# Performance work log

Hardware: AMD Instinct MI355X
Metric: run time of the kernel (lower is better)

## Reference

```python
import jax, jax.numpy as jnp
import numpy as np

B, C, H, W = 2, 64, 512, 896


def setup_inputs() -> dict:
    key = jax.random.key(0)
    k1, k2 = jax.random.split(key)
    feature = jax.random.normal(k1, (B, C, H, W), dtype=jnp.float32)
    # flow in pixel units; a few pixels of motion is typical for video frames
    flow = jax.random.normal(k2, (B, 2, H, W), dtype=jnp.float32) * 3.0
    return {"feature": feature, "flow": flow}


def reference(feature, flow):
    # Flownet2-style Resample2d: out[b,c,y,x] = bilinear(feature[b,c], y+v, x+u)
    # with zero contribution from out-of-bounds taps.
    Bv, Cv, Hv, Wv = feature.shape
    HW = Hv * Wv
    gx = flow[:, 0] + jnp.arange(Wv, dtype=flow.dtype)[None, None, :]  # [B,H,W]
    gy = flow[:, 1] + jnp.arange(Hv, dtype=flow.dtype)[None, :, None]  # [B,H,W]
    x0f = jnp.floor(gx)
    y0f = jnp.floor(gy)
    wx = gx - x0f  # frac weights
    wy = gy - y0f
    x0 = x0f.astype(jnp.int32)
    y0 = y0f.astype(jnp.int32)
    feat = feature.reshape(Bv, Cv, HW)

    def corner(xi, yi, w):
        # zero out-of-bounds taps; clip indices so the gather is always legal
        valid = (xi >= 0) & (xi < Wv) & (yi >= 0) & (yi < Hv)
        idx = jnp.clip(yi, 0, Hv - 1) * Wv + jnp.clip(xi, 0, Wv - 1)  # [B,H,W]
        idx = jnp.broadcast_to(idx.reshape(Bv, 1, HW), (Bv, Cv, HW))
        v = jnp.take_along_axis(feat, idx, axis=2)  # [B,C,HW]
        wm = (w * valid.astype(w.dtype)).reshape(Bv, 1, HW)
        return v * wm

    out = (
        corner(x0, y0, (1.0 - wx) * (1.0 - wy))
        + corner(x0 + 1, y0, wx * (1.0 - wy))
        + corner(x0, y0 + 1, (1.0 - wx) * wy)
        + corner(x0 + 1, y0 + 1, wx * wy)
    )
    return out.reshape(Bv, Cv, Hv, Wv)
```

## Files before the change

kernel.cpp:

```cpp
#include <hip/hip_runtime.h>


#define Bv 2
#define Cv 64
#define Hv 512
#define Wv 896
#define HWsz (Hv * Wv)

#define TILE 64
#define CPB 4
#define NCG (Cv / CPB)
#define SW 90
#define SH 88
#define XOFF 12
#define YOFF 11
#define NSITES (SH * SW)
#define NTX (Wv / TILE)
#define NTY (Hv / TILE)
#define NTILES (NTX * NTY)
#define NBLK (Bv * NCG * NTILES)
#define THREADS 1024
#define NW (THREADS / 64)
#define KITERS (TILE * TILE / THREADS)
#define LDS_BYTES (NSITES * CPB * 4)

__global__ __launch_bounds__(THREADS) void resample2d_kernel(
    const float* __restrict__ feature,
    const float* __restrict__ flow,
    float* __restrict__ out) {
    extern __shared__ float smem[];

    const int orig = blockIdx.x;
    const int wid = (orig & 7) * (NBLK / 8) + (orig >> 3);
    const int txi = wid % NTX;
    const int t2 = wid / NTX;
    const int tyi = t2 % NTY;
    const int zb = t2 / NTY;
    const int b = zb / NCG;
    const int c0 = (zb % NCG) * CPB;

    const int tx0 = txi * TILE;
    const int ty0 = tyi * TILE;
    const int xs = tx0 - XOFF;
    const int ys = ty0 - YOFF;

    const int tid = threadIdx.x;
    const int lane = tid & 63;
    const int wv = tid >> 6;

    const float* __restrict__ fbase = feature + ((size_t)b * Cv + c0) * HWsz;
    const float* __restrict__ flb = flow + (size_t)b * 2 * HWsz;
    float* __restrict__ ob = out + ((size_t)b * Cv + c0) * HWsz;

    const int px = tx0 + lane;
    float u[KITERS], v[KITERS];
    int pixk[KITERS];
#pragma unroll
    for (int k = 0; k < KITERS; ++k) {
        const int y = ty0 + wv + NW * k;
        pixk[k] = y * Wv + px;
        u[k] = flb[pixk[k]];
        v[k] = flb[HWsz + pixk[k]];
    }

    const bool interior = (xs >= 0) & (xs + SW <= Wv) & (ys >= 0) & (ys + SH <= Hv);
    if (interior) {
#pragma unroll
        for (int k = 0; k < 8; ++k) {
            const int p = tid + THREADS * k;
            if (p < NSITES) {
                const int r = p / SW;
                const int xx = p - r * SW;
                const float* src = fbase + (size_t)(ys + r) * Wv + (xs + xx);
                float4 val;
                val.x = src[0];
                val.y = src[HWsz];
                val.z = src[2 * HWsz];
                val.w = src[3 * HWsz];
                *(float4*)(&smem[(size_t)p * CPB]) = val;
            }
        }
    } else {
#pragma unroll
        for (int k = 0; k < 8; ++k) {
            const int p = tid + THREADS * k;
            if (p < NSITES) {
                const int r = p / SW;
                const int xx = p - r * SW;
                const int gy = ys + r;
                const int gx = xs + xx;
                float4 val = make_float4(0.0f, 0.0f, 0.0f, 0.0f);
                if (((unsigned)gy < (unsigned)Hv) & ((unsigned)gx < (unsigned)Wv)) {
                    const float* src = fbase + (size_t)gy * Wv + gx;
                    val.x = src[0];
                    val.y = src[HWsz];
                    val.z = src[2 * HWsz];
                    val.w = src[3 * HWsz];
                }
                *(float4*)(&smem[(size_t)p * CPB]) = val;
            }
        }
    }

    float w00[KITERS], w10[KITERS], w01[KITERS], w11[KITERS];
    int ac[KITERS];
    bool inwin[KITERS];
#pragma unroll
    for (int k = 0; k < KITERS; ++k) {
        const int y = ty0 + wv + NW * k;
        const float gx = u[k] + (float)px;
        const float gy = v[k] + (float)y;
        const float x0f = floorf(gx);
        const float y0f = floorf(gy);
        const float wx = gx - x0f;
        const float wy = gy - y0f;
        const float omx = 1.0f - wx;
        const float omy = 1.0f - wy;
        w00[k] = omx * omy;
        w10[k] = wx * omy;
        w01[k] = omx * wy;
        w11[k] = wx * wy;
        const int lx = (int)x0f - xs;
        const int ly = (int)y0f - ys;
        inwin[k] = ((unsigned)lx <= (unsigned)(SW - 2)) &
                   ((unsigned)ly <= (unsigned)(SH - 2));
        const int lxc = min(max(lx, 0), SW - 2);
        const int lyc = min(max(ly, 0), SH - 2);
        ac[k] = (lyc * SW + lxc) * CPB;
    }

    __syncthreads();

#define READ(T, K)                                                  \
    do {                                                            \
        const int a_ = ac[K];                                       \
        T[0] = *(const float4*)(&smem[a_]);                         \
        T[1] = *(const float4*)(&smem[a_ + CPB]);                   \
        T[2] = *(const float4*)(&smem[a_ + SW * CPB]);              \
        T[3] = *(const float4*)(&smem[a_ + SW * CPB + CPB]);        \
    } while (0)

#define CONSUME(T, K)                                                         \
    do {                                                                      \
        if (!inwin[K]) {     \
            const float gx_ = u[K] + (float)px;                               \
            const float gy_ = v[K] + (float)(ty0 + wv + NW * (K));            \
            const int x0_ = (int)floorf(gx_);                                 \
            const int y0_ = (int)floorf(gy_);                                 \
            const int x1_ = x0_ + 1, y1_ = y0_ + 1;                           \
            const bool vx0 = (unsigned)x0_ < (unsigned)Wv;                    \
            const bool vx1 = (unsigned)x1_ < (unsigned)Wv;                    \
            const bool vy0 = (unsigned)y0_ < (unsigned)Hv;                    \
            const bool vy1 = (unsigned)y1_ < (unsigned)Hv;                    \
            const int cx0 = min(max(x0_, 0), Wv - 1);                         \
            const int cx1 = min(max(x1_, 0), Wv - 1);                         \
            const int cy0 = min(max(y0_, 0), Hv - 1);                         \
            const int cy1 = min(max(y1_, 0), Hv - 1);                         \
            _Pragma("unroll") for (int c = 0; c < CPB; ++c) {                 \
                const float* f = fbase + (size_t)c * HWsz;                    \
                ((float*)&T[0])[c] = (vx0 & vy0) ? f[cy0 * Wv + cx0] : 0.0f;  \
                ((float*)&T[1])[c] = (vx1 & vy0) ? f[cy0 * Wv + cx1] : 0.0f;  \
                ((float*)&T[2])[c] = (vx0 & vy1) ? f[cy1 * Wv + cx0] : 0.0f;  \
                ((float*)&T[3])[c] = (vx1 & vy1) ? f[cy1 * Wv + cx1] : 0.0f;  \
            }                                                                 \
        }                                                                     \
        _Pragma("unroll") for (int c = 0; c < CPB; ++c) {                     \
            const float r_ = ((const float*)&T[0])[c] * w00[K] +              \
                             ((const float*)&T[1])[c] * w10[K] +              \
                             ((const float*)&T[2])[c] * w01[K] +              \
                             ((const float*)&T[3])[c] * w11[K];               \
            __builtin_nontemporal_store(r_, &ob[(size_t)c * HWsz + pixk[K]]); \
        }                                                                     \
    } while (0)

    float4 tA[4], tB[4];
    READ(tA, 0);
    READ(tB, 1);
    CONSUME(tA, 0);
    READ(tA, 2);
    CONSUME(tB, 1);
    READ(tB, 3);
    CONSUME(tA, 2);
    CONSUME(tB, 3);

#undef READ
#undef CONSUME
}

extern "C" void kernel_launch(void* const* d_in, const int* in_sizes, int n_in,
                              void* d_out, int out_size, void* d_ws, size_t ws_size,
                              hipStream_t stream) {
    const float* feature = (const float*)d_in[0];
    const float* flow = (const float*)d_in[1];
    float* out = (float*)d_out;

    static bool inited = false;
    if (!inited) {
        hipFuncSetAttribute((const void*)resample2d_kernel,
                            hipFuncAttributeMaxDynamicSharedMemorySize, LDS_BYTES);
        inited = true;
    }

    dim3 block(THREADS, 1, 1);
    dim3 grid(NBLK, 1, 1);
    resample2d_kernel<<<grid, block, LDS_BYTES, stream>>>(feature, flow, out);
}
```

Before: 467.6 us.

## Halve channels per block to shrink LDS tile and raise occupancy

Cuts channels per block from four to two, so the LDS halo tile is stored as float2 in static shared memory and each block needs half the LDS. The launch bound now asks for a minimum of 8 blocks, which pressures the compiler to cut registers. Bilinear weights are computed at consume time from wx/wy, and in-window flags are packed into a bitmask. The goal is more resident waves to hide gather and load latency. The cost is twice as many blocks, each reloading flow and recomputing coordinates and halo, and the padded stride becomes 91.

```diff
diff --git a/kernel.cpp b/kernel.cpp
--- a/kernel.cpp
+++ b/kernel.cpp
@@ -8,9 +8,9 @@
 #define HWsz (Hv * Wv)
 
 #define TILE 64
-#define CPB 4
+#define CPB 2
 #define NCG (Cv / CPB)
-#define SW 90
+#define SW 91
 #define SH 88
 #define XOFF 12
 #define YOFF 11
@@ -22,13 +22,12 @@
 #define THREADS 1024
 #define NW (THREADS / 64)
 #define KITERS (TILE * TILE / THREADS)
-#define LDS_BYTES (NSITES * CPB * 4)
 
-__global__ __launch_bounds__(THREADS) void resample2d_kernel(
+__global__ __launch_bounds__(THREADS, 8) void resample2d_kernel(
     const float* __restrict__ feature,
     const float* __restrict__ flow,
     float* __restrict__ out) {
-    extern __shared__ float smem[];
+    __shared__ float2 smem[NSITES];
 
     const int orig = blockIdx.x;
     const int wid = (orig & 7) * (NBLK / 8) + (orig >> 3);
@@ -54,13 +53,12 @@
 
     const int px = tx0 + lane;
     float u[KITERS], v[KITERS];
-    int pixk[KITERS];
 #pragma unroll
     for (int k = 0; k < KITERS; ++k) {
         const int y = ty0 + wv + NW * k;
-        pixk[k] = y * Wv + px;
-        u[k] = flb[pixk[k]];
-        v[k] = flb[HWsz + pixk[k]];
+        const int pix = y * Wv + px;
+        u[k] = flb[pix];
+        v[k] = flb[HWsz + pix];
     }
 
     const bool interior = (xs >= 0) & (xs + SW <= Wv) & (ys >= 0) & (ys + SH <= Hv);
@@ -72,12 +70,10 @@
                 const int r = p / SW;
                 const int xx = p - r * SW;
                 const float* src = fbase + (size_t)(ys + r) * Wv + (xs + xx);
-                float4 val;
+                float2 val;
                 val.x = src[0];
                 val.y = src[HWsz];
-                val.z = src[2 * HWsz];
-                val.w = src[3 * HWsz];
-                *(float4*)(&smem[(size_t)p * CPB]) = val;
+                smem[p] = val;
             }
         }
     } else {
@@ -89,22 +85,20 @@
                 const int xx = p - r * SW;
                 const int gy = ys + r;
                 const int gx = xs + xx;
-                float4 val = make_float4(0.0f, 0.0f, 0.0f, 0.0f);
+                float2 val = make_float2(0.0f, 0.0f);
                 if (((unsigned)gy < (unsigned)Hv) & ((unsigned)gx < (unsigned)Wv)) {
                     const float* src = fbase + (size_t)gy * Wv + gx;
                     val.x = src[0];
                     val.y = src[HWsz];
-                    val.z = src[2 * HWsz];
-                    val.w = src[3 * HWsz];
                 }
-                *(float4*)(&smem[(size_t)p * CPB]) = val;
+                smem[p] = val;
             }
         }
     }
 
-    float w00[KITERS], w10[KITERS], w01[KITERS], w11[KITERS];
+    float wx[KITERS], wy[KITERS];
     int ac[KITERS];
-    bool inwin[KITERS];
+    unsigned iw = 0;
 #pragma unroll
     for (int k = 0; k < KITERS; ++k) {
         const int y = ty0 + wv + NW * k;
@@ -112,68 +106,70 @@
         const float gy = v[k] + (float)y;
         const float x0f = floorf(gx);
         const float y0f = floorf(gy);
-        const float wx = gx - x0f;
-        const float wy = gy - y0f;
-        const float omx = 1.0f - wx;
-        const float omy = 1.0f - wy;
-        w00[k] = omx * omy;
-        w10[k] = wx * omy;
-        w01[k] = omx * wy;
-        w11[k] = wx * wy;
+        wx[k] = gx - x0f;
+        wy[k] = gy - y0f;
         const int lx = (int)x0f - xs;
         const int ly = (int)y0f - ys;
-        inwin[k] = ((unsigned)lx <= (unsigned)(SW - 2)) &
-                   ((unsigned)ly <= (unsigned)(SH - 2));
+        const bool inwin = ((unsigned)lx <= (unsigned)(SW - 2)) &
+                           ((unsigned)ly <= (unsigned)(SH - 2));
+        iw |= inwin ? (1u << k) : 0u;
         const int lxc = min(max(lx, 0), SW - 2);
         const int lyc = min(max(ly, 0), SH - 2);
-        ac[k] = (lyc * SW + lxc) * CPB;
+        ac[k] = lyc * SW + lxc;
     }
 
     __syncthreads();
 
-#define READ(T, K)                                                  \
-    do {                                                            \
-        const int a_ = ac[K];                                       \
-        T[0] = *(const float4*)(&smem[a_]);                         \
-        T[1] = *(const float4*)(&smem[a_ + CPB]);                   \
-        T[2] = *(const float4*)(&smem[a_ + SW * CPB]);              \
-        T[3] = *(const float4*)(&smem[a_ + SW * CPB + CPB]);        \
+#define READ(T, K)                        \
+    do {                                  \
+        const int a_ = ac[K];             \
+        T[0] = smem[a_];                  \
+        T[1] = smem[a_ + 1];              \
+        T[2] = smem[a_ + SW];             \
+        T[3] = smem[a_ + SW + 1];         \
     } while (0)
 
-#define CONSUME(T, K)                                                         \
-    do {                                                                      \
-        if (!inwin[K]) {     \
-            const float gx_ = u[K] + (float)px;                               \
-            const float gy_ = v[K] + (float)(ty0 + wv + NW * (K));            \
-            const int x0_ = (int)floorf(gx_);                                 \
-            const int y0_ = (int)floorf(gy_);                                 \
-            const int x1_ = x0_ + 1, y1_ = y0_ + 1;                           \
-            const bool vx0 = (unsigned)x0_ < (unsigned)Wv;                    \
-            const bool vx1 = (unsigned)x1_ < (unsigned)Wv;                    \
-            const bool vy0 = (unsigned)y0_ < (unsigned)Hv;                    \
-            const bool vy1 = (unsigned)y1_ < (unsigned)Hv;                    \
-            const int cx0 = min(max(x0_, 0), Wv - 1);                         \
-            const int cx1 = min(max(x1_, 0), Wv - 1);                         \
-            const int cy0 = min(max(y0_, 0), Hv - 1);                         \
-            const int cy1 = min(max(y1_, 0), Hv - 1);                         \
-            _Pragma("unroll") for (int c = 0; c < CPB; ++c) {                 \
-                const float* f = fbase + (size_t)c * HWsz;                    \
-                ((float*)&T[0])[c] = (vx0 & vy0) ? f[cy0 * Wv + cx0] : 0.0f;  \
-                ((float*)&T[1])[c] = (vx1 & vy0) ? f[cy0 * Wv + cx1] : 0.0f;  \
-                ((float*)&T[2])[c] = (vx0 & vy1) ? f[cy1 * Wv + cx0] : 0.0f;  \
-                ((float*)&T[3])[c] = (vx1 & vy1) ? f[cy1 * Wv + cx1] : 0.0f;  \
-            }                                                                 \
-        }                                                                     \
-        _Pragma("unroll") for (int c = 0; c < CPB; ++c) {                     \
-            const float r_ = ((const float*)&T[0])[c] * w00[K] +              \
-                             ((const float*)&T[1])[c] * w10[K] +              \
-                             ((const float*)&T[2])[c] * w01[K] +              \
-                             ((const float*)&T[3])[c] * w11[K];               \
-            __builtin_nontemporal_store(r_, &ob[(size_t)c * HWsz + pixk[K]]); \
-        }                                                                     \
+#define CONSUME(T, K)                                                          \
+    do {                                                                       \
+        if (!(iw & (1u << (K)))) {            \
+            const int y_ = ty0 + wv + NW * (K);                                \
+            const float gx_ = u[K] + (float)px;                                \
+            const float gy_ = v[K] + (float)y_;                                \
+            const int x0_ = (int)floorf(gx_);                                  \
+            const int y0_ = (int)floorf(gy_);                                  \
+            const int x1_ = x0_ + 1, y1_ = y0_ + 1;                            \
+            const bool vx0 = (unsigned)x0_ < (unsigned)Wv;                     \
+            const bool vx1 = (unsigned)x1_ < (unsigned)Wv;                     \
+            const bool vy0 = (unsigned)y0_ < (unsigned)Hv;                     \
+            const bool vy1 = (unsigned)y1_ < (unsigned)Hv;                     \
+            const int cx0 = min(max(x0_, 0), Wv - 1);                          \
+            const int cx1 = min(max(x1_, 0), Wv - 1);                          \
+            const int cy0 = min(max(y0_, 0), Hv - 1);                          \
+            const int cy1 = min(max(y1_, 0), Hv - 1);                          \
+            _Pragma("unroll") for (int c = 0; c < CPB; ++c) {                  \
+                const float* f = fbase + (size_t)c * HWsz;                     \
+                ((float*)&T[0])[c] = (vx0 & vy0) ? f[cy0 * Wv + cx0] : 0.0f;   \
+                ((float*)&T[1])[c] = (vx1 & vy0) ? f[cy0 * Wv + cx1] : 0.0f;   \
+                ((float*)&T[2])[c] = (vx0 & vy1) ? f[cy1 * Wv + cx0] : 0.0f;   \
+                ((float*)&T[3])[c] = (vx1 & vy1) ? f[cy1 * Wv + cx1] : 0.0f;   \
+            }                                                                  \
+        }                                                                      \
+        const float omx = 1.0f - wx[K];                                        \
+        const float omy = 1.0f - wy[K];                                        \
+        const float w00 = omx * omy;                                           \
+        const float w10 = wx[K] * omy;                                         \
+        const float w01 = omx * wy[K];                                         \
+        const float w11 = wx[K] * wy[K];                                       \
+        const int pix_ = (ty0 + wv + NW * (K)) * Wv + px;                      \
+        const float r0 = T[0].x * w00 + T[1].x * w10 +                         \
+                         T[2].x * w01 + T[3].x * w11;                          \
+        const float r1 = T[0].y * w00 + T[1].y * w10 +                         \
+                         T[2].y * w01 + T[3].y * w11;                          \
+        __builtin_nontemporal_store(r0, &ob[pix_]);                            \
+        __builtin_nontemporal_store(r1, &ob[HWsz + pix_]);                     \
     } while (0)
 
-    float4 tA[4], tB[4];
+    float2 tA[4], tB[4];
     READ(tA, 0);
     READ(tB, 1);
     CONSUME(tA, 0);
@@ -194,14 +190,7 @@
     const float* flow = (const float*)d_in[1];
     float* out = (float*)d_out;
 
-    static bool inited = false;
-    if (!inited) {
-        hipFuncSetAttribute((const void*)resample2d_kernel,
-                            hipFuncAttributeMaxDynamicSharedMemorySize, LDS_BYTES);
-        inited = true;
-    }
-
     dim3 block(THREADS, 1, 1);
     dim3 grid(NBLK, 1, 1);
-    resample2d_kernel<<<grid, block, LDS_BYTES, stream>>>(feature, flow, out);
+    resample2d_kernel<<<grid, block, 0, stream>>>(feature, flow, out);
 }
```

After: 428.2 us. 1.09x faster.
